# Kernel tuning notes

Measured on AMD Instinct MI355X. Metric: run time of the kernel, lower is better.

The kernel has to match this reference:

```python
import jax, jax.numpy as jnp
import numpy as np
import math

DIM = 256
N = 4096
E = 1024
NEG = -1.0e9


def setup_inputs() -> dict:
    key = jax.random.key(0)
    ks = jax.random.split(key, 10)
    x = jax.random.normal(ks[0], (N, DIM), dtype=jnp.float32)
    # sparse incidence / adjacency (module only uses >0 as mask)
    H = (jax.random.uniform(ks[1], (N, E)) < 0.05).astype(jnp.float32)
    adj = (jax.random.uniform(ks[2], (N, N)) < 0.01).astype(jnp.float32)
    s = 1.0 / math.sqrt(DIM)
    W_he = jax.random.normal(ks[3], (DIM, DIM), dtype=jnp.float32) * s  # HyperedgeAttention.W
    u = jax.random.normal(ks[4], (DIM,), dtype=jnp.float32)            # HyperedgeAttention.u
    W_e = jax.random.normal(ks[5], (DIM, DIM), dtype=jnp.float32) * s  # NodeAttention.W_e
    W_n = jax.random.normal(ks[6], (DIM, DIM), dtype=jnp.float32) * s  # NodeAttention.W_n
    W_g = jax.random.normal(ks[7], (DIM, DIM), dtype=jnp.float32) * s  # GraphAttention.W
    a_g = jax.random.normal(ks[8], (2 * DIM,), dtype=jnp.float32) * s  # GraphAttention.attn weight
    return {"x": x, "H": H, "adj": adj, "W_he": W_he, "u": u,
            "W_e": W_e, "W_n": W_n, "W_g": W_g, "a_g": a_g}


def reference(x, H, adj, W_he, u, W_e, W_n, W_g, a_g):
    n, dim = x.shape
    inv_sqrt_d = 1.0 / math.sqrt(dim)
    maskH = H > 0                       # [N,E] bool
    mask_Hf = maskH.astype(x.dtype)

    # ---- HyperedgeAttention ----
    h_he = x @ W_he                     # [N,dim]
    sc = (h_he @ u) * inv_sqrt_d        # [N]
    scE = jnp.where(maskH, sc[:, None], NEG)      # [N,E]
    A = jax.nn.softmax(scE, axis=0) * mask_Hf     # column softmax over nodes
    e_repr = A.T @ h_he                 # [E,dim]

    # ---- NodeAttention (only B is used) ----
    hn = x @ W_n                        # [N,dim]
    he = e_repr @ W_e                   # [E,dim]
    Bsc = jnp.where(maskH, (hn @ he.T) * inv_sqrt_d, NEG)
    B = jax.nn.softmax(Bsc, axis=1) * mask_Hf     # [N,E]

    # ---- GraphAttention (concat score split: e_ij = lrelu(h_i.a1 + h_j.a2)) ----
    h_g = x @ W_g                       # [N,dim]
    s1 = h_g @ a_g[:dim]                # [N]
    s2 = h_g @ a_g[dim:]                # [N]
    e = jax.nn.leaky_relu(s1[:, None] + s2[None, :], 0.2)   # [N,N]
    maskA = (adj > 0).astype(x.dtype)
    sl = jnp.eye(n, dtype=x.dtype)
    e = e * (maskA + sl) - 1e9 * jnp.clip(1.0 - maskA - sl, 0.0, None)
    G = jax.nn.softmax(e, axis=1)       # [N,N]

    # ---- Mixing ----
    he_sz = jnp.clip(mask_Hf.sum(0), 1.0, None)   # [E]
    M = (G @ mask_Hf) / he_sz[None, :]            # [N,E]
    A_hat = jax.nn.softmax(A.T + M.T, axis=1) * mask_Hf.T   # [E,N]
    e_mix = A_hat @ (x @ W_he)                    # [E,dim]
    B_hat = jax.nn.softmax(B + M, axis=1) * mask_Hf          # [N,E]
    z_h = jax.nn.elu(B_hat @ (e_mix @ W_e))       # [N,dim]
    G_hat = jax.nn.softmax(G + B @ B.T + A @ A.T, axis=1)    # [N,N]
    z_g = jax.nn.elu(G_hat @ (x @ W_g))           # [N,dim]
    return z_h, z_g
```

## Files before the change

### kernel.cpp

```cpp
#include <hip/hip_runtime.h>
#include <math.h>
#include <stdint.h>

#define Nn 4096
#define Ee 1024
#define Dd 256

typedef __attribute__((ext_vector_type(8))) __bf16 bf16x8;
typedef __attribute__((ext_vector_type(4))) float f32x4;
typedef __attribute__((ext_vector_type(8))) unsigned short u16x8;

__device__ __forceinline__ unsigned short f2bf(float f) {
  unsigned int u = __float_as_uint(f);
  unsigned int r = (u + 0x7fffu + ((u >> 16) & 1u)) >> 16;
  return (unsigned short)r;
}
__device__ __forceinline__ float bf2f(unsigned short u) {
  return __uint_as_float(((unsigned int)u) << 16);
}

__device__ __forceinline__ void gload_lds16(const void* g, void* l) {
  __builtin_amdgcn_global_load_lds(
      (__attribute__((address_space(1))) void*)const_cast<void*>(g),
      (__attribute__((address_space(3))) void*)l, 16, 0, 0);
}

__device__ __forceinline__ float block_reduce_sum(float v) {
  __shared__ float sh[4];
  #pragma unroll
  for (int o = 32; o > 0; o >>= 1) v += __shfl_down(v, o);
  int lane = threadIdx.x & 63, w = threadIdx.x >> 6;
  if (lane == 0) sh[w] = v;
  __syncthreads();
  float s = sh[0] + sh[1] + sh[2] + sh[3];
  __syncthreads();
  return s;
}

__global__ __launch_bounds__(256) void gemm_bt_bf16(
    const unsigned short* __restrict__ Ab, const unsigned short* __restrict__ Bb,
    float* __restrict__ Cp, unsigned short* __restrict__ Cb,
    int M, int N, int K, int lda, int ldb, float alpha)
{
  __shared__ unsigned short As[2][128 * 32];
  __shared__ unsigned short Bs[2][128 * 32];
  const int tid = threadIdx.x;
  const int m0 = blockIdx.x * 128, n0 = blockIdx.y * 128;
  const int wave = tid >> 6, lane = tid & 63;
  const int wr = (wave >> 1) * 64, wc = (wave & 1) * 64;
  const int l16 = lane & 15, lq = lane >> 4;
  f32x4 acc[4][4] = {};
  const int NT = K >> 5;

  auto stage = [&](int buf, int kt) {
    const int k0 = kt * 32;
    #pragma unroll
    for (int i = 0; i < 2; ++i) {
      int t2 = tid + i * 256;
      int r = t2 >> 2, c = (t2 & 3) * 8;
      gload_lds16(Ab + (size_t)(m0 + r) * lda + k0 + c, &As[buf][t2 * 8]);
    }
    #pragma unroll
    for (int i = 0; i < 2; ++i) {
      int t2 = tid + i * 256;
      int r = t2 >> 2, c = (t2 & 3) * 8;
      gload_lds16(Bb + (size_t)(n0 + r) * ldb + k0 + c, &Bs[buf][t2 * 8]);
    }
  };

  stage(0, 0);
  __syncthreads();
  int buf = 0;
  for (int kt = 0; kt < NT; ++kt) {
    if (kt + 1 < NT) stage(buf ^ 1, kt + 1);
    bf16x8 af[4], bfr[4];
    #pragma unroll
    for (int m = 0; m < 4; ++m)
      af[m] = *reinterpret_cast<const bf16x8*>(&As[buf][(wr + m * 16 + l16) * 32 + lq * 8]);
    #pragma unroll
    for (int n = 0; n < 4; ++n)
      bfr[n] = *reinterpret_cast<const bf16x8*>(&Bs[buf][(wc + n * 16 + l16) * 32 + lq * 8]);
    #pragma unroll
    for (int m = 0; m < 4; ++m)
      #pragma unroll
      for (int n = 0; n < 4; ++n)
        acc[m][n] = __builtin_amdgcn_mfma_f32_16x16x32_bf16(af[m], bfr[n], acc[m][n], 0, 0, 0);
    __syncthreads();
    buf ^= 1;
  }
  #pragma unroll
  for (int m = 0; m < 4; ++m)
    #pragma unroll
    for (int n = 0; n < 4; ++n) {
      int col = n0 + wc + n * 16 + l16;
      #pragma unroll
      for (int q = 0; q < 4; ++q) {
        int row = m0 + wr + m * 16 + lq * 4 + q;
        size_t idx = (size_t)row * N + col;
        float v = acc[m][n][q] * alpha;
        Cp[idx] = v;
        if (Cb) Cb[idx] = f2bf(v);
      }
    }
}

__global__ __launch_bounds__(256) void gemm_bts_bf16(
    const unsigned short* __restrict__ Ab, const unsigned short* __restrict__ Bb,
    float* __restrict__ Cp, int M, int N, int K, int lda, int ldb, int KS)
{
  __shared__ unsigned short As[2][128 * 32];
  __shared__ unsigned short Bs[2][128 * 32];
  const int tid = threadIdx.x;
  const int m0 = blockIdx.x * 128, n0 = blockIdx.y * 128;
  const int kbase = blockIdx.z * KS;
  const int wave = tid >> 6, lane = tid & 63;
  const int wr = (wave >> 1) * 64, wc = (wave & 1) * 64;
  const int l16 = lane & 15, lq = lane >> 4;
  f32x4 acc[4][4] = {};
  const int NT = KS >> 5;

  auto stage = [&](int buf, int kt) {
    const int k0 = kbase + kt * 32;
    #pragma unroll
    for (int i = 0; i < 2; ++i) {
      int t2 = tid + i * 256;
      int r = t2 >> 2, c = (t2 & 3) * 8;
      gload_lds16(Ab + (size_t)(m0 + r) * lda + k0 + c, &As[buf][t2 * 8]);
    }
    #pragma unroll
    for (int i = 0; i < 2; ++i) {
      int t2 = tid + i * 256;
      int r = t2 >> 2, c = (t2 & 3) * 8;
      gload_lds16(Bb + (size_t)(n0 + r) * ldb + k0 + c, &Bs[buf][t2 * 8]);
    }
  };

  stage(0, 0);
  __syncthreads();
  int buf = 0;
  for (int kt = 0; kt < NT; ++kt) {
    if (kt + 1 < NT) stage(buf ^ 1, kt + 1);
    bf16x8 af[4], bfr[4];
    #pragma unroll
    for (int m = 0; m < 4; ++m)
      af[m] = *reinterpret_cast<const bf16x8*>(&As[buf][(wr + m * 16 + l16) * 32 + lq * 8]);
    #pragma unroll
    for (int n = 0; n < 4; ++n)
      bfr[n] = *reinterpret_cast<const bf16x8*>(&Bs[buf][(wc + n * 16 + l16) * 32 + lq * 8]);
    #pragma unroll
    for (int m = 0; m < 4; ++m)
      #pragma unroll
      for (int n = 0; n < 4; ++n)
        acc[m][n] = __builtin_amdgcn_mfma_f32_16x16x32_bf16(af[m], bfr[n], acc[m][n], 0, 0, 0);
    __syncthreads();
    buf ^= 1;
  }
  #pragma unroll
  for (int m = 0; m < 4; ++m)
    #pragma unroll
    for (int n = 0; n < 4; ++n) {
      int col = n0 + wc + n * 16 + l16;
      #pragma unroll
      for (int q = 0; q < 4; ++q) {
        int row = m0 + wr + m * 16 + lq * 4 + q;
        atomicAdd(&Cp[(size_t)row * N + col], acc[m][n][q]);
      }
    }
}

__global__ __launch_bounds__(256) void gemm_gram_k(
    const unsigned short* __restrict__ CAT,
    unsigned short* __restrict__ Gb,
    float* __restrict__ rowsum)
{
  const int bx = blockIdx.x, by = blockIdx.y;
  if (bx > by) return;
  const int K = 2048;
  __shared__ unsigned short SM[17024];
  unsigned short* Asb = SM;
  unsigned short* Bsb = SM + 8192;
  const int tid = threadIdx.x;
  const int m0 = bx * 128, n0 = by * 128;
  const int wave = tid >> 6, lane = tid & 63;
  const int wr = (wave >> 1) * 64, wc = (wave & 1) * 64;
  const int l16 = lane & 15, lq = lane >> 4;
  f32x4 acc[4][4] = {};
  const int NT = K >> 5;

  auto stage = [&](int buf, int kt) {
    const int k0 = kt * 32;
    #pragma unroll
    for (int i = 0; i < 2; ++i) {
      int t2 = tid + i * 256;
      int r = t2 >> 2, c = (t2 & 3) * 8;
      gload_lds16(CAT + (size_t)(m0 + r) * K + k0 + c, Asb + buf * 4096 + t2 * 8);
    }
    #pragma unroll
    for (int i = 0; i < 2; ++i) {
      int t2 = tid + i * 256;
      int r = t2 >> 2, c = (t2 & 3) * 8;
      gload_lds16(CAT + (size_t)(n0 + r) * K + k0 + c, Bsb + buf * 4096 + t2 * 8);
    }
  };

  stage(0, 0);
  __syncthreads();
  int buf = 0;
  for (int kt = 0; kt < NT; ++kt) {
    if (kt + 1 < NT) stage(buf ^ 1, kt + 1);
    bf16x8 af[4], bfr[4];
    #pragma unroll
    for (int m = 0; m < 4; ++m)
      af[m] = *reinterpret_cast<const bf16x8*>(Asb + buf * 4096 + (wr + m * 16 + l16) * 32 + lq * 8);
    #pragma unroll
    for (int n = 0; n < 4; ++n)
      bfr[n] = *reinterpret_cast<const bf16x8*>(Bsb + buf * 4096 + (wc + n * 16 + l16) * 32 + lq * 8);
    #pragma unroll
    for (int m = 0; m < 4; ++m)
      #pragma unroll
      for (int n = 0; n < 4; ++n)
        acc[m][n] = __builtin_amdgcn_mfma_f32_16x16x32_bf16(af[m], bfr[n], acc[m][n], 0, 0, 0);
    __syncthreads();
    buf ^= 1;
  }
  #pragma unroll
  for (int m = 0; m < 4; ++m)
    #pragma unroll
    for (int q = 0; q < 4; ++q) {
      int row = m0 + wr + m * 16 + lq * 4 + q;
      float s = 0.f;
      #pragma unroll
      for (int n = 0; n < 4; ++n) {
        int col = n0 + wc + n * 16 + l16;
        size_t idx = (size_t)row * Nn + col;
        float e = expf(bf2f(Gb[idx]) + acc[m][n][q]);
        Gb[idx] = f2bf(e);
        s += e;
      }
      s += __shfl_xor(s, 1); s += __shfl_xor(s, 2);
      s += __shfl_xor(s, 4); s += __shfl_xor(s, 8);
      if (l16 == 0) atomicAdd(&rowsum[row], s);
    }
  if (bx == by) return;

  __syncthreads();
  unsigned short* Tg = SM;
  {
    int cc = tid >> 1, r0 = (tid & 1) * 64;
    const unsigned short* src = Gb + (size_t)(n0 + cc) * Nn + m0 + r0;
    unsigned short* dst = Tg + cc * 132 + r0;
    #pragma unroll
    for (int v = 0; v < 8; ++v)
      *reinterpret_cast<u16x8*>(dst + v * 8) = *reinterpret_cast<const u16x8*>(src + v * 8);
  }
  __syncthreads();
  #pragma unroll
  for (int n = 0; n < 4; ++n) {
    int ccl = wc + n * 16 + l16;
    float cs = 0.f;
    #pragma unroll
    for (int m = 0; m < 4; ++m) {
      int sa = ccl * 132 + wr + m * 16 + lq * 4;
      ushort4 lg = *reinterpret_cast<const ushort4*>(&Tg[sa]);
      ushort4 eo;
      float e0 = expf(bf2f(lg.x) + acc[m][n][0]); eo.x = f2bf(e0); cs += e0;
      float e1 = expf(bf2f(lg.y) + acc[m][n][1]); eo.y = f2bf(e1); cs += e1;
      float e2 = expf(bf2f(lg.z) + acc[m][n][2]); eo.z = f2bf(e2); cs += e2;
      float e3 = expf(bf2f(lg.w) + acc[m][n][3]); eo.w = f2bf(e3); cs += e3;
      *reinterpret_cast<ushort4*>(&Tg[sa]) = eo;
    }
    cs += __shfl_xor(cs, 16); cs += __shfl_xor(cs, 32);
    if (lq == 0) atomicAdd(&rowsum[n0 + ccl], cs);
  }
  __syncthreads();
  {
    int cc = tid >> 1, r0 = (tid & 1) * 64;
    const unsigned short* src = Tg + cc * 132 + r0;
    unsigned short* dst = Gb + (size_t)(n0 + cc) * Nn + m0 + r0;
    #pragma unroll
    for (int v = 0; v < 8; ++v)
      *reinterpret_cast<u16x8*>(dst + v * 8) = *reinterpret_cast<const u16x8*>(src + v * 8);
  }
}

__global__ __launch_bounds__(256) void gemm64s_bt_bf16(
    const unsigned short* __restrict__ Ab, const unsigned short* __restrict__ Bb,
    float* __restrict__ Cp, int M, int N, int K, int KS)
{
  __shared__ unsigned short As[2][64 * 64];
  __shared__ unsigned short Bs[2][64 * 64];
  const int tid = threadIdx.x;
  const int m0 = blockIdx.x * 64, n0 = blockIdx.y * 64;
  const int kbase = blockIdx.z * KS;
  const int wave = tid >> 6, lane = tid & 63;
  const int wr = (wave >> 1) * 32, wc = (wave & 1) * 32;
  const int l16 = lane & 15, lq = lane >> 4;
  f32x4 acc[2][2] = {};
  const int NT = KS >> 6;

  auto stage = [&](int buf, int kt) {
    const int k0 = kbase + kt * 64;
    #pragma unroll
    for (int i = 0; i < 2; ++i) {
      int t2 = tid + i * 256;
      int r = t2 >> 3, c = (t2 & 7) * 8;
      gload_lds16(Ab + (size_t)(m0 + r) * K + k0 + c, &As[buf][t2 * 8]);
    }
    #pragma unroll
    for (int i = 0; i < 2; ++i) {
      int t2 = tid + i * 256;
      int r = t2 >> 3, c = (t2 & 7) * 8;
      gload_lds16(Bb + (size_t)(n0 + r) * K + k0 + c, &Bs[buf][t2 * 8]);
    }
  };

  stage(0, 0);
  __syncthreads();
  int buf = 0;
  for (int kt = 0; kt < NT; ++kt) {
    if (kt + 1 < NT) stage(buf ^ 1, kt + 1);
    bf16x8 af[2][2], bfr[2][2];
    #pragma unroll
    for (int m = 0; m < 2; ++m)
      #pragma unroll
      for (int ks = 0; ks < 2; ++ks)
        af[m][ks] = *reinterpret_cast<const bf16x8*>(
            &As[buf][(wr + m * 16 + l16) * 64 + ks * 32 + lq * 8]);
    #pragma unroll
    for (int n = 0; n < 2; ++n)
      #pragma unroll
      for (int ks = 0; ks < 2; ++ks)
        bfr[n][ks] = *reinterpret_cast<const bf16x8*>(
            &Bs[buf][(wc + n * 16 + l16) * 64 + ks * 32 + lq * 8]);
    #pragma unroll
    for (int m = 0; m < 2; ++m)
      #pragma unroll
      for (int n = 0; n < 2; ++n)
        #pragma unroll
        for (int ks = 0; ks < 2; ++ks)
          acc[m][n] = __builtin_amdgcn_mfma_f32_16x16x32_bf16(af[m][ks], bfr[n][ks], acc[m][n], 0, 0, 0);
    __syncthreads();
    buf ^= 1;
  }
  #pragma unroll
  for (int m = 0; m < 2; ++m)
    #pragma unroll
    for (int n = 0; n < 2; ++n) {
      int col = n0 + wc + n * 16 + l16;
      #pragma unroll
      for (int q = 0; q < 4; ++q) {
        int row = m0 + wr + m * 16 + lq * 4 + q;
        atomicAdd(&Cp[(size_t)row * N + col], acc[m][n][q]);
      }
    }
}

__global__ __launch_bounds__(256) void cvt_bf16_k(const float* __restrict__ in,
                                                  unsigned short* __restrict__ out, long n) {
  long i = ((long)blockIdx.x * 256 + threadIdx.x) * 8;
  if (i + 8 > n) return;
  float4 a = *reinterpret_cast<const float4*>(&in[i]);
  float4 b = *reinterpret_cast<const float4*>(&in[i + 4]);
  u16x8 o;
  o[0] = f2bf(a.x); o[1] = f2bf(a.y); o[2] = f2bf(a.z); o[3] = f2bf(a.w);
  o[4] = f2bf(b.x); o[5] = f2bf(b.y); o[6] = f2bf(b.z); o[7] = f2bf(b.w);
  *reinterpret_cast<u16x8*>(&out[i]) = o;
}

__global__ __launch_bounds__(256) void tcvt_k(const float* __restrict__ in,
                                              unsigned short* __restrict__ outT, int R, int S,
                                              const float* __restrict__ coldiv) {
  __shared__ unsigned short tile[64][65];
  int r0 = blockIdx.x * 64, c0 = blockIdx.y * 64;
  int t = threadIdx.x & 63, q = threadIdx.x >> 6;
  float sc = coldiv ? 1.f / fmaxf(coldiv[c0 + t], 1.f) : 1.f;
  for (int rr = q; rr < 64; rr += 4)
    tile[t][rr] = f2bf(in[(long)(r0 + rr) * S + c0 + t] * sc);
  __syncthreads();
  for (int cc = q; cc < 64; cc += 4)
    outT[(long)(c0 + cc) * R + r0 + t] = tile[cc][t];
}

__global__ __launch_bounds__(256) void tcvtW_k(const float* __restrict__ W0,
                                               const float* __restrict__ W1,
                                               const float* __restrict__ W2,
                                               const float* __restrict__ W3,
                                               unsigned short* __restrict__ outT) {
  __shared__ unsigned short tile[64][65];
  int s = blockIdx.z;
  const float* in = s == 0 ? W0 : (s == 1 ? W1 : (s == 2 ? W2 : W3));
  unsigned short* o = outT + (size_t)s * 256 * 256;
  int r0 = blockIdx.x * 64, c0 = blockIdx.y * 64;
  int t = threadIdx.x & 63, q = threadIdx.x >> 6;
  for (int rr = q; rr < 64; rr += 4)
    tile[t][rr] = f2bf(in[(long)(r0 + rr) * Dd + c0 + t]);
  __syncthreads();
  for (int cc = q; cc < 64; cc += 4)
    o[(long)(c0 + cc) * Dd + r0 + t] = tile[cc][t];
}

__global__ __launch_bounds__(256) void tcvtH_k(const float* __restrict__ hcat4,
                                               unsigned short* __restrict__ hWT,
                                               unsigned short* __restrict__ hgT) {
  __shared__ unsigned short tile[64][65];
  int s = blockIdx.z;
  const float* in = hcat4 + (s == 0 ? 768 : 512);
  unsigned short* o = s == 0 ? hWT : hgT;
  int r0 = blockIdx.x * 64, c0 = blockIdx.y * 64;
  int t = threadIdx.x & 63, q = threadIdx.x >> 6;
  for (int rr = q; rr < 64; rr += 4)
    tile[t][rr] = f2bf(in[(long)(r0 + rr) * 1024 + c0 + t]);
  __syncthreads();
  for (int cc = q; cc < 64; cc += 4)
    o[(long)(c0 + cc) * Nn + r0 + t] = tile[cc][t];
}

__global__ __launch_bounds__(256) void elu_rows_k(float* __restrict__ p,
                                                  const float* __restrict__ rowsum) {
  long i = ((long)blockIdx.x * 256 + threadIdx.x) * 4;
  float4 v = *reinterpret_cast<const float4*>(&p[i]);
  float sc = 1.f;
  long half = (long)Nn * Dd;
  if (i >= half) sc = 1.f / rowsum[(i - half) >> 8];
  v.x *= sc; v.y *= sc; v.z *= sc; v.w *= sc;
  v.x = v.x > 0.f ? v.x : expm1f(v.x);
  v.y = v.y > 0.f ? v.y : expm1f(v.y);
  v.z = v.z > 0.f ? v.z : expm1f(v.z);
  v.w = v.w > 0.f ? v.w : expm1f(v.w);
  *reinterpret_cast<float4*>(&p[i]) = v;
}

__global__ __launch_bounds__(256) void gemm64_k(
    const float* __restrict__ Ap, const float* __restrict__ Bp, float* __restrict__ Cp,
    int M, int N, int K, int Asm, int Ask, int Bsk, int Bsn)
{
  __shared__ alignas(16) float As[16][68];
  __shared__ alignas(16) float Bs[16][68];
  const int tid = threadIdx.x;
  const int tx = tid & 15, ty = tid >> 4;
  const int m0 = blockIdx.x * 64, n0 = blockIdx.y * 64;
  float acc[4][4] = {};
  for (int k0 = 0; k0 < K; k0 += 16) {
    if (Ask == 1) {
      int mm = tid >> 2, kk = (tid & 3) << 2;
      float4 v = *reinterpret_cast<const float4*>(&Ap[(long)(m0 + mm) * Asm + k0 + kk]);
      As[kk + 0][mm] = v.x; As[kk + 1][mm] = v.y; As[kk + 2][mm] = v.z; As[kk + 3][mm] = v.w;
    } else {
      int kk = tid >> 4, mm = (tid & 15) << 2;
      *reinterpret_cast<float4*>(&As[kk][mm]) =
          *reinterpret_cast<const float4*>(&Ap[(long)(k0 + kk) * Ask + m0 + mm]);
    }
    if (Bsn == 1) {
      int kk = tid >> 4, nn = (tid & 15) << 2;
      *reinterpret_cast<float4*>(&Bs[kk][nn]) =
          *reinterpret_cast<const float4*>(&Bp[(long)(k0 + kk) * Bsk + n0 + nn]);
    } else {
      int nn = tid >> 2, kk = (tid & 3) << 2;
      float4 v = *reinterpret_cast<const float4*>(&Bp[(long)(n0 + nn) * Bsn + k0 + kk]);
      Bs[kk + 0][nn] = v.x; Bs[kk + 1][nn] = v.y; Bs[kk + 2][nn] = v.z; Bs[kk + 3][nn] = v.w;
    }
    __syncthreads();
    #pragma unroll
    for (int kk = 0; kk < 16; ++kk) {
      float4 av = *reinterpret_cast<const float4*>(&As[kk][ty << 2]);
      float4 bv = *reinterpret_cast<const float4*>(&Bs[kk][tx << 2]);
      float a[4] = {av.x, av.y, av.z, av.w};
      float b[4] = {bv.x, bv.y, bv.z, bv.w};
      #pragma unroll
      for (int r = 0; r < 4; ++r)
        #pragma unroll
        for (int c = 0; c < 4; ++c) acc[r][c] = fmaf(a[r], b[c], acc[r][c]);
    }
    __syncthreads();
  }
  #pragma unroll
  for (int r = 0; r < 4; ++r) {
    long base = (long)(m0 + (ty << 2) + r) * N + n0 + (tx << 2);
    float4 o = {acc[r][0], acc[r][1], acc[r][2], acc[r][3]};
    *reinterpret_cast<float4*>(&Cp[base]) = o;
  }
}

__global__ __launch_bounds__(256) void rowdots_k(
    const float* __restrict__ hcat, const float* __restrict__ u, const float* __restrict__ a_g,
    float* __restrict__ esc, float* __restrict__ s1, float* __restrict__ s2)
{
  int i = blockIdx.x, t = threadIdx.x;
  float hh = hcat[(long)i * 1024 + t];
  float hg = hcat[(long)i * 1024 + 512 + t];
  float d0 = block_reduce_sum(hh * u[t]);
  float d1 = block_reduce_sum(hg * a_g[t]);
  float d2 = block_reduce_sum(hg * a_g[Dd + t]);
  if (t == 0) {
    esc[i] = expf(d0 * 0.0625f);
    s1[i] = d1;
    s2[i] = d2;
  }
}

__global__ __launch_bounds__(256) void colstats_k(
    const float* __restrict__ H, const float* __restrict__ esc,
    float* __restrict__ colden, float* __restrict__ cnt)
{
  int e = blockIdx.x * 256 + threadIdx.x;
  int r0 = blockIdx.y * 128;
  float d = 0.f, c = 0.f;
  for (int r = r0; r < r0 + 128; ++r) {
    float h = H[(long)r * Ee + e];
    if (h > 0.f) { d += esc[r]; c += 1.f; }
  }
  atomicAdd(&colden[e], d);
  atomicAdd(&cnt[e], c);
}

__global__ __launch_bounds__(256) void fillA_k(
    const float* __restrict__ H, const float* __restrict__ esc,
    const float* __restrict__ colden,
    unsigned short* __restrict__ CAT, unsigned short* __restrict__ AbT)
{
  __shared__ unsigned short tile[64][68];
  int r0 = blockIdx.x * 64, e0 = blockIdx.y * 64;
  int te = threadIdx.x & 63, tq = threadIdx.x >> 6;
  float cd = colden[e0 + te];
  for (int rr = tq; rr < 64; rr += 4) {
    long idx = (long)(r0 + rr) * Ee + e0 + te;
    float h = H[idx];
    float val = h > 0.f ? esc[r0 + rr] / cd : 0.f;
    unsigned short vb = f2bf(val);
    CAT[(long)(r0 + rr) * 2048 + 1024 + e0 + te] = vb;
    tile[te][rr] = vb;
  }
  __syncthreads();
  for (int ee = tq; ee < 64; ee += 4)
    AbT[(long)(e0 + ee) * Nn + r0 + te] = tile[ee][te];
}

__global__ __launch_bounds__(256) void brow_k(const float* __restrict__ Bbuf,
                                              const float* __restrict__ H,
                                              unsigned short* __restrict__ CAT)
{
  int i = blockIdx.x, t = threadIdx.x;
  long base = (long)i * Ee + t * 4;
  float4 raw = *reinterpret_cast<const float4*>(&Bbuf[base]);
  float4 h = *reinterpret_cast<const float4*>(&H[base]);
  float rr[4] = {raw.x, raw.y, raw.z, raw.w}, hh[4] = {h.x, h.y, h.z, h.w};
  float p[4]; float s = 0.f;
  #pragma unroll
  for (int k = 0; k < 4; ++k) { p[k] = hh[k] > 0.f ? expf(rr[k]) : 0.f; s += p[k]; }
  float den = block_reduce_sum(s);
  float inv = den > 0.f ? 1.f / den : 0.f;
  ushort4 ob = {f2bf(p[0] * inv), f2bf(p[1] * inv), f2bf(p[2] * inv), f2bf(p[3] * inv)};
  *reinterpret_cast<ushort4*>(&CAT[(long)i * 2048 + t * 4]) = ob;
}

__global__ __launch_bounds__(256) void gfill_k(
    const float* __restrict__ adj, const float* __restrict__ s1,
    const float* __restrict__ s2, unsigned short* __restrict__ Gb)
{
  int i = blockIdx.x, t = threadIdx.x;
  float s1i = s1[i];
  float p[16]; float sum = 0.f;
  #pragma unroll
  for (int c = 0; c < 4; ++c) {
    int j = c * 1024 + t * 4;
    float4 a = *reinterpret_cast<const float4*>(&adj[(long)i * Nn + j]);
    float4 sv = *reinterpret_cast<const float4*>(&s2[j]);
    float aa[4] = {a.x, a.y, a.z, a.w}, ss[4] = {sv.x, sv.y, sv.z, sv.w};
    #pragma unroll
    for (int k = 0; k < 4; ++k) {
      float f = (aa[k] > 0.f ? 1.f : 0.f) + ((j + k) == i ? 1.f : 0.f);
      float l = s1i + ss[k];
      l = l > 0.f ? l : 0.2f * l;
      float val = l * f - 1e9f * fmaxf(1.f - f, 0.f);
      float pp = expf(val);
      p[c * 4 + k] = pp; sum += pp;
    }
  }
  float den = block_reduce_sum(sum);
  float inv = 1.f / den;
  #pragma unroll
  for (int c = 0; c < 4; ++c) {
    int j = c * 1024 + t * 4;
    ushort4 ob = {f2bf(p[c * 4] * inv), f2bf(p[c * 4 + 1] * inv),
                  f2bf(p[c * 4 + 2] * inv), f2bf(p[c * 4 + 3] * inv)};
    *reinterpret_cast<ushort4*>(&Gb[(long)i * Nn + j]) = ob;
  }
}

__global__ __launch_bounds__(256) void amstats_k(
    const unsigned short* __restrict__ CAT, const float* __restrict__ Mm,
    float* __restrict__ aden)
{
  int e = blockIdx.x * 256 + threadIdx.x;
  int r0 = blockIdx.y * 128;
  float d = 0.f;
  for (int r = r0; r < r0 + 128; ++r)
    d += expf(bf2f(CAT[(size_t)r * 2048 + 1024 + e]) + Mm[(size_t)r * Ee + e]);
  atomicAdd(&aden[e], d);
}

__global__ __launch_bounds__(256) void ahat_k(
    const unsigned short* __restrict__ CAT, const float* __restrict__ Mm,
    const float* __restrict__ H, const float* __restrict__ aden,
    unsigned short* __restrict__ AhB)
{
  __shared__ float tile[64][65];
  int j0 = blockIdx.x * 64, e0 = blockIdx.y * 64;
  int te = threadIdx.x & 63;
  int tq = threadIdx.x >> 6;
  int e = e0 + te;
  float inv = 1.f / aden[e];
  for (int jj = tq; jj < 64; jj += 4) {
    long idx = (long)(j0 + jj) * Ee + e;
    float a = bf2f(CAT[(size_t)(j0 + jj) * 2048 + 1024 + e]);
    float val = (H[idx] > 0.f) ? expf(a + Mm[idx]) * inv : 0.f;
    tile[te][jj] = val;
  }
  __syncthreads();
  for (int ee = tq; ee < 64; ee += 4)
    AhB[(long)(e0 + ee) * Nn + j0 + te] = f2bf(tile[ee][te]);
}

__global__ __launch_bounds__(256) void bhat_k(const unsigned short* __restrict__ CAT,
                                              const float* __restrict__ Mm,
                                              const float* __restrict__ H,
                                              unsigned short* __restrict__ Bb2)
{
  int i = blockIdx.x, t = threadIdx.x;
  long base = (long)i * Ee + t * 4;
  ushort4 bu = *reinterpret_cast<const ushort4*>(&CAT[(long)i * 2048 + t * 4]);
  float4 m = *reinterpret_cast<const float4*>(&Mm[base]);
  float4 h = *reinterpret_cast<const float4*>(&H[base]);
  float bb[4] = {bf2f(bu.x), bf2f(bu.y), bf2f(bu.z), bf2f(bu.w)};
  float mm2[4] = {m.x, m.y, m.z, m.w}, hh[4] = {h.x, h.y, h.z, h.w};
  float p[4]; float s = 0.f;
  #pragma unroll
  for (int k = 0; k < 4; ++k) { p[k] = expf(bb[k] + mm2[k]); s += p[k]; }
  float den = block_reduce_sum(s);
  float inv = 1.f / den;
  #pragma unroll
  for (int k = 0; k < 4; ++k) p[k] = hh[k] > 0.f ? p[k] * inv : 0.f;
  ushort4 ob = {f2bf(p[0]), f2bf(p[1]), f2bf(p[2]), f2bf(p[3])};
  *reinterpret_cast<ushort4*>(&Bb2[base]) = ob;
}

extern "C" void kernel_launch(void* const* d_in, const int* in_sizes, int n_in,
                              void* d_out, int out_size, void* d_ws, size_t ws_size,
                              hipStream_t stream) {
  const float* x    = (const float*)d_in[0];
  const float* H    = (const float*)d_in[1];
  const float* adj  = (const float*)d_in[2];
  const float* W_he = (const float*)d_in[3];
  const float* u    = (const float*)d_in[4];
  const float* W_e  = (const float*)d_in[5];
  const float* W_n  = (const float*)d_in[6];
  const float* W_g  = (const float*)d_in[7];
  const float* a_g  = (const float*)d_in[8];
  float* out = (float*)d_out;
  float* ws  = (float*)d_ws;
  (void)in_sizes; (void)n_in; (void)out_size; (void)ws_size;

  size_t off = 0;
  auto alloc = [&](size_t n) { float* p = ws + off; off += n; return p; };
  float* hcat4  = alloc((size_t)Nn * 1024);
  float* Wp     = alloc((size_t)Dd * Dd);
  float* esc    = alloc(Nn);
  float* s1     = alloc(Nn);
  float* s2     = alloc(Nn);
  float* colden = alloc(Ee);
  float* cnt    = alloc(Ee);
  float* aden   = alloc(Ee);
  float* rowsum = alloc(Nn);
  float* heb    = alloc((size_t)Ee * Dd);
  float* tewTf  = alloc((size_t)Dd * Ee);
  float* Bbuf   = alloc((size_t)Nn * Ee);
  float* Mm     = alloc((size_t)Nn * Ee);
  unsigned short* Gb    = (unsigned short*)alloc((size_t)Nn * Nn / 2);
  unsigned short* CAT   = (unsigned short*)alloc((size_t)Nn * 2048 / 2);
  unsigned short* Hbt   = (unsigned short*)alloc((size_t)Ee * Nn / 2);
  unsigned short* AbT   = (unsigned short*)alloc((size_t)Ee * Nn / 2);
  unsigned short* AhB   = (unsigned short*)alloc((size_t)Ee * Nn / 2);
  unsigned short* hWT   = (unsigned short*)alloc((size_t)Dd * Nn / 2);
  unsigned short* hgT   = (unsigned short*)alloc((size_t)Dd * Nn / 2);
  unsigned short* tewT  = (unsigned short*)alloc((size_t)Dd * Ee / 2);
  unsigned short* Bb2   = (unsigned short*)alloc((size_t)Nn * Ee / 2);
  unsigned short* xb    = (unsigned short*)alloc((size_t)Nn * Dd / 2);
  unsigned short* WcTb4 = (unsigned short*)alloc((size_t)1024 * Dd / 2);
  unsigned short* hcatB = (unsigned short*)alloc((size_t)Nn * 1024 / 2);
  unsigned short* hebB  = (unsigned short*)alloc((size_t)Ee * Dd / 2);

  hipMemsetAsync(colden, 0, (3 * Ee + Nn) * sizeof(float), stream);
  hipMemsetAsync(heb, 0, 2 * (size_t)Ee * Dd * sizeof(float), stream);
  hipMemsetAsync(Mm, 0, (size_t)Nn * Ee * sizeof(float), stream);
  hipMemsetAsync(out, 0, 2 * (size_t)Nn * Dd * sizeof(float), stream);

  auto gbt = [&](const unsigned short* A, const unsigned short* B, float* C, unsigned short* Cb,
                 int M, int N, int K, int lda, int ldb, float alpha) {
    gemm_bt_bf16<<<dim3(M / 128, N / 128), 256, 0, stream>>>(A, B, C, Cb, M, N, K, lda, ldb, alpha);
  };
  auto gbts = [&](const unsigned short* A, const unsigned short* B, float* C,
                  int M, int N, int K, int lda, int ldb, int KS) {
    gemm_bts_bf16<<<dim3(M / 128, N / 128, K / KS), 256, 0, stream>>>(A, B, C, M, N, K, lda, ldb, KS);
  };
  auto gs64 = [&](const unsigned short* A, const unsigned short* B, float* C,
                  int M, int N, int K, int KS) {
    gemm64s_bt_bf16<<<dim3(M / 64, N / 64, K / KS), 256, 0, stream>>>(A, B, C, M, N, K, KS);
  };
  auto tcvt = [&](const float* in, unsigned short* o, int R, int S, int cols, const float* cd) {
    tcvt_k<<<dim3(R / 64, cols / 64), 256, 0, stream>>>(in, o, R, S, cd);
  };

  gemm64_k<<<dim3(4, 4), 256, 0, stream>>>(W_he, W_e, Wp, Dd, Dd, Dd, Dd, 1, Dd, 1);
  cvt_bf16_k<<<(Nn * Dd) / 2048, 256, 0, stream>>>(x, xb, (long)Nn * Dd);
  tcvtW_k<<<dim3(4, 4, 4), 256, 0, stream>>>(W_he, W_n, W_g, Wp, WcTb4);
  gbt(xb, WcTb4, hcat4, hcatB, Nn, 1024, Dd, Dd, Dd, 1.f);
  rowdots_k<<<Nn, 256, 0, stream>>>(hcat4, u, a_g, esc, s1, s2);
  tcvtH_k<<<dim3(Nn / 64, Dd / 64, 2), 256, 0, stream>>>(hcat4, hWT, hgT);
  colstats_k<<<dim3(Ee / 256, 32), 256, 0, stream>>>(H, esc, colden, cnt);
  fillA_k<<<dim3(Nn / 64, Ee / 64), 256, 0, stream>>>(H, esc, colden, CAT, AbT);
  gs64(AbT, hWT, heb, Ee, Dd, Nn, 512);
  cvt_bf16_k<<<(Ee * Dd) / 2048, 256, 0, stream>>>(heb, hebB, (long)Ee * Dd);
  gbt(hcatB + 256, hebB, Bbuf, nullptr, Nn, Ee, Dd, 1024, Dd, 0.0625f);
  brow_k<<<Nn, 256, 0, stream>>>(Bbuf, H, CAT);
  gfill_k<<<Nn, 256, 0, stream>>>(adj, s1, s2, Gb);
  tcvt(H, Hbt, Nn, Ee, Ee, cnt);
  gbts(Gb, Hbt, Mm, Nn, Ee, Nn, Nn, Nn, 2048);
  gemm_gram_k<<<dim3(32, 32), 256, 0, stream>>>(CAT, Gb, rowsum);
  amstats_k<<<dim3(Ee / 256, 32), 256, 0, stream>>>(CAT, Mm, aden);
  ahat_k<<<dim3(Nn / 64, Ee / 64), 256, 0, stream>>>(CAT, Mm, H, aden, AhB);
  gs64(hWT, AhB, tewTf, Dd, Ee, Nn, 512);
  cvt_bf16_k<<<(Dd * Ee) / 2048, 256, 0, stream>>>(tewTf, tewT, (long)Dd * Ee);
  bhat_k<<<Nn, 256, 0, stream>>>(CAT, Mm, H, Bb2);
  gs64(Bb2, tewT, out, Nn, Dd, Ee, 512);
  gbts(Gb, hgT, out + (size_t)Nn * Dd, Nn, Dd, Nn, Nn, Nn, 512);
  elu_rows_k<<<(2 * Nn * Dd) / 1024, 256, 0, stream>>>(out, rowsum);
}
```

Measured before the change: 592.2 us.

## Merge independent GEMMs into combined launches and defer softmax normalisations

The G@H GEMM and the Gram/exp kernel now run in one launch, using separate z-slices and a separate Gexp output buffer so that Gb stays readable. The z_g GEMM and the hWT·AhB GEMM are likewise packed into one launch. The A-hat and B-hat softmax denominators are no longer applied in place. They are folded into a tew conversion (division by aden) and into the final ELU scaling (bden), and a new expbm kernel computes B-hat and the A column sums in a single pass. The aim is fewer launches and fewer serialized stages, with better GPU fill from co-scheduling. The cost is an extra N×N bf16 buffer and a heavier expbm block loop.

```diff
diff --git a/kernel.cpp b/kernel.cpp
--- a/kernel.cpp
+++ b/kernel.cpp
@@ -35,6 +35,215 @@
   float s = sh[0] + sh[1] + sh[2] + sh[3];
   __syncthreads();
   return s;
+}
+
+__device__ __forceinline__ void bts_dev(
+    const unsigned short* __restrict__ Ab, const unsigned short* __restrict__ Bb,
+    float* __restrict__ Cp, int N, int lda, int ldb,
+    int m0, int n0, int kbase, int NT, unsigned short* SM)
+{
+  unsigned short* As = SM;
+  unsigned short* Bs = SM + 8192;
+  const int tid = threadIdx.x;
+  const int wave = tid >> 6, lane = tid & 63;
+  const int wr = (wave >> 1) * 64, wc = (wave & 1) * 64;
+  const int l16 = lane & 15, lq = lane >> 4;
+  f32x4 acc[4][4] = {};
+
+  auto stage = [&](int buf, int kt) {
+    const int k0 = kbase + kt * 32;
+    #pragma unroll
+    for (int i = 0; i < 2; ++i) {
+      int t2 = tid + i * 256;
+      int r = t2 >> 2, c = (t2 & 3) * 8;
+      gload_lds16(Ab + (size_t)(m0 + r) * lda + k0 + c, As + buf * 4096 + t2 * 8);
+    }
+    #pragma unroll
+    for (int i = 0; i < 2; ++i) {
+      int t2 = tid + i * 256;
+      int r = t2 >> 2, c = (t2 & 3) * 8;
+      gload_lds16(Bb + (size_t)(n0 + r) * ldb + k0 + c, Bs + buf * 4096 + t2 * 8);
+    }
+  };
+
+  stage(0, 0);
+  __syncthreads();
+  int buf = 0;
+  for (int kt = 0; kt < NT; ++kt) {
+    if (kt + 1 < NT) stage(buf ^ 1, kt + 1);
+    bf16x8 af[4], bfr[4];
+    #pragma unroll
+    for (int m = 0; m < 4; ++m)
+      af[m] = *reinterpret_cast<const bf16x8*>(As + buf * 4096 + (wr + m * 16 + l16) * 32 + lq * 8);
+    #pragma unroll
+    for (int n = 0; n < 4; ++n)
+      bfr[n] = *reinterpret_cast<const bf16x8*>(Bs + buf * 4096 + (wc + n * 16 + l16) * 32 + lq * 8);
+    #pragma unroll
+    for (int m = 0; m < 4; ++m)
+      #pragma unroll
+      for (int n = 0; n < 4; ++n)
+        acc[m][n] = __builtin_amdgcn_mfma_f32_16x16x32_bf16(af[m], bfr[n], acc[m][n], 0, 0, 0);
+    __syncthreads();
+    buf ^= 1;
+  }
+  #pragma unroll
+  for (int m = 0; m < 4; ++m)
+    #pragma unroll
+    for (int n = 0; n < 4; ++n) {
+      int col = n0 + wc + n * 16 + l16;
+      #pragma unroll
+      for (int q = 0; q < 4; ++q) {
+        int row = m0 + wr + m * 16 + lq * 4 + q;
+        atomicAdd(&Cp[(size_t)row * N + col], acc[m][n][q]);
+      }
+    }
+}
+
+__device__ __forceinline__ void gram_dev(
+    const unsigned short* __restrict__ CAT, const unsigned short* __restrict__ Gb,
+    unsigned short* __restrict__ Gexp, float* __restrict__ rowsum,
+    int bx, int by, unsigned short* SM)
+{
+  const int K = 2048;
+  unsigned short* Asb = SM;
+  unsigned short* Bsb = SM + 8192;
+  const int tid = threadIdx.x;
+  const int m0 = bx * 128, n0 = by * 128;
+  const int wave = tid >> 6, lane = tid & 63;
+  const int wr = (wave >> 1) * 64, wc = (wave & 1) * 64;
+  const int l16 = lane & 15, lq = lane >> 4;
+  f32x4 acc[4][4] = {};
+  const int NT = K >> 5;
+
+  auto stage = [&](int buf, int kt) {
+    const int k0 = kt * 32;
+    #pragma unroll
+    for (int i = 0; i < 2; ++i) {
+      int t2 = tid + i * 256;
+      int r = t2 >> 2, c = (t2 & 3) * 8;
+      gload_lds16(CAT + (size_t)(m0 + r) * K + k0 + c, Asb + buf * 4096 + t2 * 8);
+    }
+    #pragma unroll
+    for (int i = 0; i < 2; ++i) {
+      int t2 = tid + i * 256;
+      int r = t2 >> 2, c = (t2 & 3) * 8;
+      gload_lds16(CAT + (size_t)(n0 + r) * K + k0 + c, Bsb + buf * 4096 + t2 * 8);
+    }
+  };
+
+  stage(0, 0);
+  __syncthreads();
+  int buf = 0;
+  for (int kt = 0; kt < NT; ++kt) {
+    if (kt + 1 < NT) stage(buf ^ 1, kt + 1);
+    bf16x8 af[4], bfr[4];
+    #pragma unroll
+    for (int m = 0; m < 4; ++m)
+      af[m] = *reinterpret_cast<const bf16x8*>(Asb + buf * 4096 + (wr + m * 16 + l16) * 32 + lq * 8);
+    #pragma unroll
+    for (int n = 0; n < 4; ++n)
+      bfr[n] = *reinterpret_cast<const bf16x8*>(Bsb + buf * 4096 + (wc + n * 16 + l16) * 32 + lq * 8);
+    #pragma unroll
+    for (int m = 0; m < 4; ++m)
+      #pragma unroll
+      for (int n = 0; n < 4; ++n)
+        acc[m][n] = __builtin_amdgcn_mfma_f32_16x16x32_bf16(af[m], bfr[n], acc[m][n], 0, 0, 0);
+    __syncthreads();
+    buf ^= 1;
+  }
+  #pragma unroll
+  for (int m = 0; m < 4; ++m)
+    #pragma unroll
+    for (int q = 0; q < 4; ++q) {
+      int row = m0 + wr + m * 16 + lq * 4 + q;
+      float s = 0.f;
+      #pragma unroll
+      for (int n = 0; n < 4; ++n) {
+        int col = n0 + wc + n * 16 + l16;
+        size_t idx = (size_t)row * Nn + col;
+        float e = expf(bf2f(Gb[idx]) + acc[m][n][q]);
+        Gexp[idx] = f2bf(e);
+        s += e;
+      }
+      s += __shfl_xor(s, 1); s += __shfl_xor(s, 2);
+      s += __shfl_xor(s, 4); s += __shfl_xor(s, 8);
+      if (l16 == 0) atomicAdd(&rowsum[row], s);
+    }
+  if (bx == by) return;
+
+  __syncthreads();
+  unsigned short* Tg = SM;
+  {
+    int cc = tid >> 1, r0 = (tid & 1) * 64;
+    const unsigned short* src = Gb + (size_t)(n0 + cc) * Nn + m0 + r0;
+    unsigned short* dst = Tg + cc * 132 + r0;
+    #pragma unroll
+    for (int v = 0; v < 8; ++v)
+      *reinterpret_cast<u16x8*>(dst + v * 8) = *reinterpret_cast<const u16x8*>(src + v * 8);
+  }
+  __syncthreads();
+  #pragma unroll
+  for (int n = 0; n < 4; ++n) {
+    int ccl = wc + n * 16 + l16;
+    float cs = 0.f;
+    #pragma unroll
+    for (int m = 0; m < 4; ++m) {
+      int sa = ccl * 132 + wr + m * 16 + lq * 4;
+      ushort4 lg = *reinterpret_cast<const ushort4*>(&Tg[sa]);
+      ushort4 eo;
+      float e0 = expf(bf2f(lg.x) + acc[m][n][0]); eo.x = f2bf(e0); cs += e0;
+      float e1 = expf(bf2f(lg.y) + acc[m][n][1]); eo.y = f2bf(e1); cs += e1;
+      float e2 = expf(bf2f(lg.z) + acc[m][n][2]); eo.z = f2bf(e2); cs += e2;
+      float e3 = expf(bf2f(lg.w) + acc[m][n][3]); eo.w = f2bf(e3); cs += e3;
+      *reinterpret_cast<ushort4*>(&Tg[sa]) = eo;
+    }
+    cs += __shfl_xor(cs, 16); cs += __shfl_xor(cs, 32);
+    if (lq == 0) atomicAdd(&rowsum[n0 + ccl], cs);
+  }
+  __syncthreads();
+  {
+    int cc = tid >> 1, r0 = (tid & 1) * 64;
+    const unsigned short* src = Tg + cc * 132 + r0;
+    unsigned short* dst = Gexp + (size_t)(n0 + cc) * Nn + m0 + r0;
+    #pragma unroll
+    for (int v = 0; v < 8; ++v)
+      *reinterpret_cast<u16x8*>(dst + v * 8) = *reinterpret_cast<const u16x8*>(src + v * 8);
+  }
+}
+
+__global__ __launch_bounds__(256) void mgram_k(
+    const unsigned short* __restrict__ CAT, const unsigned short* __restrict__ Gb,
+    unsigned short* __restrict__ Gexp, float* __restrict__ rowsum,
+    const unsigned short* __restrict__ Hbt, float* __restrict__ Mm)
+{
+  __shared__ unsigned short SM[17024];
+  if (blockIdx.z == 0) {
+    if (blockIdx.x > blockIdx.y) return;
+    gram_dev(CAT, Gb, Gexp, rowsum, blockIdx.x, blockIdx.y, SM);
+  } else {
+    int m0 = blockIdx.x * 128;
+    int n0 = (blockIdx.y & 7) * 128;
+    int kbase = (blockIdx.y >> 3) * 1024;
+    bts_dev(Gb, Hbt, Mm, Ee, Nn, Nn, m0, n0, kbase, 32, SM);
+  }
+}
+
+__global__ __launch_bounds__(256) void zgtew_k(
+    const unsigned short* __restrict__ Gexp, const unsigned short* __restrict__ hgT,
+    float* __restrict__ outzg,
+    const unsigned short* __restrict__ hWT, const unsigned short* __restrict__ AhB,
+    float* __restrict__ tewTf)
+{
+  __shared__ unsigned short SM[16384];
+  int z = blockIdx.z;
+  if (z < 8) {
+    bts_dev(Gexp, hgT, outzg, Dd, Nn, Nn, blockIdx.x * 128, blockIdx.y * 128, z * 512, 16, SM);
+  } else {
+    int linear = (z - 8) * 64 + blockIdx.y * 32 + blockIdx.x;
+    int tile = linear & 15, ks = linear >> 4;
+    int m0 = (tile >> 3) * 128, n0 = (tile & 7) * 128;
+    bts_dev(hWT, AhB, tewTf, Ee, Nn, Nn, m0, n0, ks * 512, 16, SM);
+  }
 }
 
 __global__ __launch_bounds__(256) void gemm_bt_bf16(
@@ -102,185 +311,6 @@
         if (Cb) Cb[idx] = f2bf(v);
       }
     }
-}
-
-__global__ __launch_bounds__(256) void gemm_bts_bf16(
-    const unsigned short* __restrict__ Ab, const unsigned short* __restrict__ Bb,
-    float* __restrict__ Cp, int M, int N, int K, int lda, int ldb, int KS)
-{
-  __shared__ unsigned short As[2][128 * 32];
-  __shared__ unsigned short Bs[2][128 * 32];
-  const int tid = threadIdx.x;
-  const int m0 = blockIdx.x * 128, n0 = blockIdx.y * 128;
-  const int kbase = blockIdx.z * KS;
-  const int wave = tid >> 6, lane = tid & 63;
-  const int wr = (wave >> 1) * 64, wc = (wave & 1) * 64;
-  const int l16 = lane & 15, lq = lane >> 4;
-  f32x4 acc[4][4] = {};
-  const int NT = KS >> 5;
-
-  auto stage = [&](int buf, int kt) {
-    const int k0 = kbase + kt * 32;
-    #pragma unroll
-    for (int i = 0; i < 2; ++i) {
-      int t2 = tid + i * 256;
-      int r = t2 >> 2, c = (t2 & 3) * 8;
-      gload_lds16(Ab + (size_t)(m0 + r) * lda + k0 + c, &As[buf][t2 * 8]);
-    }
-    #pragma unroll
-    for (int i = 0; i < 2; ++i) {
-      int t2 = tid + i * 256;
-      int r = t2 >> 2, c = (t2 & 3) * 8;
-      gload_lds16(Bb + (size_t)(n0 + r) * ldb + k0 + c, &Bs[buf][t2 * 8]);
-    }
-  };
-
-  stage(0, 0);
-  __syncthreads();
-  int buf = 0;
-  for (int kt = 0; kt < NT; ++kt) {
-    if (kt + 1 < NT) stage(buf ^ 1, kt + 1);
-    bf16x8 af[4], bfr[4];
-    #pragma unroll
-    for (int m = 0; m < 4; ++m)
-      af[m] = *reinterpret_cast<const bf16x8*>(&As[buf][(wr + m * 16 + l16) * 32 + lq * 8]);
-    #pragma unroll
-    for (int n = 0; n < 4; ++n)
-      bfr[n] = *reinterpret_cast<const bf16x8*>(&Bs[buf][(wc + n * 16 + l16) * 32 + lq * 8]);
-    #pragma unroll
-    for (int m = 0; m < 4; ++m)
-      #pragma unroll
-      for (int n = 0; n < 4; ++n)
-        acc[m][n] = __builtin_amdgcn_mfma_f32_16x16x32_bf16(af[m], bfr[n], acc[m][n], 0, 0, 0);
-    __syncthreads();
-    buf ^= 1;
-  }
-  #pragma unroll
-  for (int m = 0; m < 4; ++m)
-    #pragma unroll
-    for (int n = 0; n < 4; ++n) {
-      int col = n0 + wc + n * 16 + l16;
-      #pragma unroll
-      for (int q = 0; q < 4; ++q) {
-        int row = m0 + wr + m * 16 + lq * 4 + q;
-        atomicAdd(&Cp[(size_t)row * N + col], acc[m][n][q]);
-      }
-    }
-}
-
-__global__ __launch_bounds__(256) void gemm_gram_k(
-    const unsigned short* __restrict__ CAT,
-    unsigned short* __restrict__ Gb,
-    float* __restrict__ rowsum)
-{
-  const int bx = blockIdx.x, by = blockIdx.y;
-  if (bx > by) return;
-  const int K = 2048;
-  __shared__ unsigned short SM[17024];
-  unsigned short* Asb = SM;
-  unsigned short* Bsb = SM + 8192;
-  const int tid = threadIdx.x;
-  const int m0 = bx * 128, n0 = by * 128;
-  const int wave = tid >> 6, lane = tid & 63;
-  const int wr = (wave >> 1) * 64, wc = (wave & 1) * 64;
-  const int l16 = lane & 15, lq = lane >> 4;
-  f32x4 acc[4][4] = {};
-  const int NT = K >> 5;
-
-  auto stage = [&](int buf, int kt) {
-    const int k0 = kt * 32;
-    #pragma unroll
-    for (int i = 0; i < 2; ++i) {
-      int t2 = tid + i * 256;
-      int r = t2 >> 2, c = (t2 & 3) * 8;
-      gload_lds16(CAT + (size_t)(m0 + r) * K + k0 + c, Asb + buf * 4096 + t2 * 8);
-    }
-    #pragma unroll
-    for (int i = 0; i < 2; ++i) {
-      int t2 = tid + i * 256;
-      int r = t2 >> 2, c = (t2 & 3) * 8;
-      gload_lds16(CAT + (size_t)(n0 + r) * K + k0 + c, Bsb + buf * 4096 + t2 * 8);
-    }
-  };
-
-  stage(0, 0);
-  __syncthreads();
-  int buf = 0;
-  for (int kt = 0; kt < NT; ++kt) {
-    if (kt + 1 < NT) stage(buf ^ 1, kt + 1);
-    bf16x8 af[4], bfr[4];
-    #pragma unroll
-    for (int m = 0; m < 4; ++m)
-      af[m] = *reinterpret_cast<const bf16x8*>(Asb + buf * 4096 + (wr + m * 16 + l16) * 32 + lq * 8);
-    #pragma unroll
-    for (int n = 0; n < 4; ++n)
-      bfr[n] = *reinterpret_cast<const bf16x8*>(Bsb + buf * 4096 + (wc + n * 16 + l16) * 32 + lq * 8);
-    #pragma unroll
-    for (int m = 0; m < 4; ++m)
-      #pragma unroll
-      for (int n = 0; n < 4; ++n)
-        acc[m][n] = __builtin_amdgcn_mfma_f32_16x16x32_bf16(af[m], bfr[n], acc[m][n], 0, 0, 0);
-    __syncthreads();
-    buf ^= 1;
-  }
-  #pragma unroll
-  for (int m = 0; m < 4; ++m)
-    #pragma unroll
-    for (int q = 0; q < 4; ++q) {
-      int row = m0 + wr + m * 16 + lq * 4 + q;
-      float s = 0.f;
-      #pragma unroll
-      for (int n = 0; n < 4; ++n) {
-        int col = n0 + wc + n * 16 + l16;
-        size_t idx = (size_t)row * Nn + col;
-        float e = expf(bf2f(Gb[idx]) + acc[m][n][q]);
-        Gb[idx] = f2bf(e);
-        s += e;
-      }
-      s += __shfl_xor(s, 1); s += __shfl_xor(s, 2);
-      s += __shfl_xor(s, 4); s += __shfl_xor(s, 8);
-      if (l16 == 0) atomicAdd(&rowsum[row], s);
-    }
-  if (bx == by) return;
-
-  __syncthreads();
-  unsigned short* Tg = SM;
-  {
-    int cc = tid >> 1, r0 = (tid & 1) * 64;
-    const unsigned short* src = Gb + (size_t)(n0 + cc) * Nn + m0 + r0;
-    unsigned short* dst = Tg + cc * 132 + r0;
-    #pragma unroll
-    for (int v = 0; v < 8; ++v)
-      *reinterpret_cast<u16x8*>(dst + v * 8) = *reinterpret_cast<const u16x8*>(src + v * 8);
-  }
-  __syncthreads();
-  #pragma unroll
-  for (int n = 0; n < 4; ++n) {
-    int ccl = wc + n * 16 + l16;
-    float cs = 0.f;
-    #pragma unroll
-    for (int m = 0; m < 4; ++m) {
-      int sa = ccl * 132 + wr + m * 16 + lq * 4;
-      ushort4 lg = *reinterpret_cast<const ushort4*>(&Tg[sa]);
-      ushort4 eo;
-      float e0 = expf(bf2f(lg.x) + acc[m][n][0]); eo.x = f2bf(e0); cs += e0;
-      float e1 = expf(bf2f(lg.y) + acc[m][n][1]); eo.y = f2bf(e1); cs += e1;
-      float e2 = expf(bf2f(lg.z) + acc[m][n][2]); eo.z = f2bf(e2); cs += e2;
-      float e3 = expf(bf2f(lg.w) + acc[m][n][3]); eo.w = f2bf(e3); cs += e3;
-      *reinterpret_cast<ushort4*>(&Tg[sa]) = eo;
-    }
-    cs += __shfl_xor(cs, 16); cs += __shfl_xor(cs, 32);
-    if (lq == 0) atomicAdd(&rowsum[n0 + ccl], cs);
-  }
-  __syncthreads();
-  {
-    int cc = tid >> 1, r0 = (tid & 1) * 64;
-    const unsigned short* src = Tg + cc * 132 + r0;
-    unsigned short* dst = Gb + (size_t)(n0 + cc) * Nn + m0 + r0;
-    #pragma unroll
-    for (int v = 0; v < 8; ++v)
-      *reinterpret_cast<u16x8*>(dst + v * 8) = *reinterpret_cast<const u16x8*>(src + v * 8);
-  }
 }
 
 __global__ __launch_bounds__(256) void gemm64s_bt_bf16(
@@ -364,6 +394,21 @@
   u16x8 o;
   o[0] = f2bf(a.x); o[1] = f2bf(a.y); o[2] = f2bf(a.z); o[3] = f2bf(a.w);
   o[4] = f2bf(b.x); o[5] = f2bf(b.y); o[6] = f2bf(b.z); o[7] = f2bf(b.w);
+  *reinterpret_cast<u16x8*>(&out[i]) = o;
+}
+
+__global__ __launch_bounds__(256) void cvt_cs_k(const float* __restrict__ in,
+                                                unsigned short* __restrict__ out,
+                                                const float* __restrict__ aden) {
+  long i = ((long)blockIdx.x * 256 + threadIdx.x) * 8;
+  int e0 = (int)(i & 1023);
+  float4 a = *reinterpret_cast<const float4*>(&in[i]);
+  float4 b = *reinterpret_cast<const float4*>(&in[i + 4]);
+  float4 d0 = *reinterpret_cast<const float4*>(&aden[e0]);
+  float4 d1 = *reinterpret_cast<const float4*>(&aden[e0 + 4]);
+  u16x8 o;
+  o[0] = f2bf(a.x / d0.x); o[1] = f2bf(a.y / d0.y); o[2] = f2bf(a.z / d0.z); o[3] = f2bf(a.w / d0.w);
+  o[4] = f2bf(b.x / d1.x); o[5] = f2bf(b.y / d1.y); o[6] = f2bf(b.z / d1.z); o[7] = f2bf(b.w / d1.w);
   *reinterpret_cast<u16x8*>(&out[i]) = o;
 }
 
@@ -416,12 +461,12 @@
 }
 
 __global__ __launch_bounds__(256) void elu_rows_k(float* __restrict__ p,
+                                                  const float* __restrict__ bden,
                                                   const float* __restrict__ rowsum) {
   long i = ((long)blockIdx.x * 256 + threadIdx.x) * 4;
   float4 v = *reinterpret_cast<const float4*>(&p[i]);
-  float sc = 1.f;
   long half = (long)Nn * Dd;
-  if (i >= half) sc = 1.f / rowsum[(i - half) >> 8];
+  float sc = (i < half) ? 1.f / bden[i >> 8] : 1.f / rowsum[(i - half) >> 8];
   v.x *= sc; v.y *= sc; v.z *= sc; v.w *= sc;
   v.x = v.x > 0.f ? v.x : expm1f(v.x);
   v.y = v.y > 0.f ? v.y : expm1f(v.y);
@@ -587,61 +632,59 @@
   }
 }
 
-__global__ __launch_bounds__(256) void amstats_k(
+__global__ __launch_bounds__(256) void expbm_k(
     const unsigned short* __restrict__ CAT, const float* __restrict__ Mm,
-    float* __restrict__ aden)
-{
-  int e = blockIdx.x * 256 + threadIdx.x;
-  int r0 = blockIdx.y * 128;
-  float d = 0.f;
-  for (int r = r0; r < r0 + 128; ++r)
-    d += expf(bf2f(CAT[(size_t)r * 2048 + 1024 + e]) + Mm[(size_t)r * Ee + e]);
-  atomicAdd(&aden[e], d);
+    const float* __restrict__ H, unsigned short* __restrict__ Bb2,
+    float* __restrict__ bden, float* __restrict__ aden)
+{
+  int t = threadIdx.x;
+  int i0 = blockIdx.x * 16;
+  float pa[4] = {0.f, 0.f, 0.f, 0.f};
+  for (int r = 0; r < 16; ++r) {
+    int i = i0 + r;
+    long base = (long)i * Ee + t * 4;
+    ushort4 bu = *reinterpret_cast<const ushort4*>(&CAT[(long)i * 2048 + t * 4]);
+    ushort4 au = *reinterpret_cast<const ushort4*>(&CAT[(long)i * 2048 + 1024 + t * 4]);
+    float4 m = *reinterpret_cast<const float4*>(&Mm[base]);
+    float4 h = *reinterpret_cast<const float4*>(&H[base]);
+    float mm[4] = {m.x, m.y, m.z, m.w}, hh[4] = {h.x, h.y, h.z, h.w};
+    unsigned short bs[4] = {bu.x, bu.y, bu.z, bu.w}, as[4] = {au.x, au.y, au.z, au.w};
+    float eb[4]; float s = 0.f;
+    #pragma unroll
+    for (int k = 0; k < 4; ++k) {
+      eb[k] = expf(bf2f(bs[k]) + mm[k]); s += eb[k];
+      pa[k] += expf(bf2f(as[k]) + mm[k]);
+    }
+    float den = block_reduce_sum(s);
+    ushort4 ob = {hh[0] > 0.f ? f2bf(eb[0]) : (unsigned short)0,
+                  hh[1] > 0.f ? f2bf(eb[1]) : (unsigned short)0,
+                  hh[2] > 0.f ? f2bf(eb[2]) : (unsigned short)0,
+                  hh[3] > 0.f ? f2bf(eb[3]) : (unsigned short)0};
+    *reinterpret_cast<ushort4*>(&Bb2[base]) = ob;
+    if (t == 0) bden[i] = den;
+  }
+  #pragma unroll
+  for (int k = 0; k < 4; ++k) atomicAdd(&aden[t * 4 + k], pa[k]);
 }
 
 __global__ __launch_bounds__(256) void ahat_k(
     const unsigned short* __restrict__ CAT, const float* __restrict__ Mm,
-    const float* __restrict__ H, const float* __restrict__ aden,
-    unsigned short* __restrict__ AhB)
+    const float* __restrict__ H, unsigned short* __restrict__ AhB)
 {
   __shared__ float tile[64][65];
   int j0 = blockIdx.x * 64, e0 = blockIdx.y * 64;
   int te = threadIdx.x & 63;
   int tq = threadIdx.x >> 6;
   int e = e0 + te;
-  float inv = 1.f / aden[e];
   for (int jj = tq; jj < 64; jj += 4) {
     long idx = (long)(j0 + jj) * Ee + e;
     float a = bf2f(CAT[(size_t)(j0 + jj) * 2048 + 1024 + e]);
-    float val = (H[idx] > 0.f) ? expf(a + Mm[idx]) * inv : 0.f;
+    float val = (H[idx] > 0.f) ? expf(a + Mm[idx]) : 0.f;
     tile[te][jj] = val;
   }
   __syncthreads();
   for (int ee = tq; ee < 64; ee += 4)
     AhB[(long)(e0 + ee) * Nn + j0 + te] = f2bf(tile[ee][te]);
-}
-
-__global__ __launch_bounds__(256) void bhat_k(const unsigned short* __restrict__ CAT,
-                                              const float* __restrict__ Mm,
-                                              const float* __restrict__ H,
-                                              unsigned short* __restrict__ Bb2)
-{
-  int i = blockIdx.x, t = threadIdx.x;
-  long base = (long)i * Ee + t * 4;
-  ushort4 bu = *reinterpret_cast<const ushort4*>(&CAT[(long)i * 2048 + t * 4]);
-  float4 m = *reinterpret_cast<const float4*>(&Mm[base]);
-  float4 h = *reinterpret_cast<const float4*>(&H[base]);
-  float bb[4] = {bf2f(bu.x), bf2f(bu.y), bf2f(bu.z), bf2f(bu.w)};
-  float mm2[4] = {m.x, m.y, m.z, m.w}, hh[4] = {h.x, h.y, h.z, h.w};
-  float p[4]; float s = 0.f;
-  #pragma unroll
-  for (int k = 0; k < 4; ++k) { p[k] = expf(bb[k] + mm2[k]); s += p[k]; }
-  float den = block_reduce_sum(s);
-  float inv = 1.f / den;
-  #pragma unroll
-  for (int k = 0; k < 4; ++k) p[k] = hh[k] > 0.f ? p[k] * inv : 0.f;
-  ushort4 ob = {f2bf(p[0]), f2bf(p[1]), f2bf(p[2]), f2bf(p[3])};
-  *reinterpret_cast<ushort4*>(&Bb2[base]) = ob;
 }
 
 extern "C" void kernel_launch(void* const* d_in, const int* in_sizes, int n_in,
@@ -671,11 +714,13 @@
   float* cnt    = alloc(Ee);
   float* aden   = alloc(Ee);
   float* rowsum = alloc(Nn);
+  float* bden   = alloc(Nn);
   float* heb    = alloc((size_t)Ee * Dd);
   float* tewTf  = alloc((size_t)Dd * Ee);
   float* Bbuf   = alloc((size_t)Nn * Ee);
   float* Mm     = alloc((size_t)Nn * Ee);
   unsigned short* Gb    = (unsigned short*)alloc((size_t)Nn * Nn / 2);
+  unsigned short* Gexp  = (unsigned short*)alloc((size_t)Nn * Nn / 2);
   unsigned short* CAT   = (unsigned short*)alloc((size_t)Nn * 2048 / 2);
   unsigned short* Hbt   = (unsigned short*)alloc((size_t)Ee * Nn / 2);
   unsigned short* AbT   = (unsigned short*)alloc((size_t)Ee * Nn / 2);
@@ -689,7 +734,7 @@
   unsigned short* hcatB = (unsigned short*)alloc((size_t)Nn * 1024 / 2);
   unsigned short* hebB  = (unsigned short*)alloc((size_t)Ee * Dd / 2);
 
-  hipMemsetAsync(colden, 0, (3 * Ee + Nn) * sizeof(float), stream);
+  hipMemsetAsync(colden, 0, (3 * Ee + 2 * Nn) * sizeof(float), stream);
   hipMemsetAsync(heb, 0, 2 * (size_t)Ee * Dd * sizeof(float), stream);
   hipMemsetAsync(Mm, 0, (size_t)Nn * Ee * sizeof(float), stream);
   hipMemsetAsync(out, 0, 2 * (size_t)Nn * Dd * sizeof(float), stream);
@@ -697,10 +742,6 @@
   auto gbt = [&](const unsigned short* A, const unsigned short* B, float* C, unsigned short* Cb,
                  int M, int N, int K, int lda, int ldb, float alpha) {
     gemm_bt_bf16<<<dim3(M / 128, N / 128), 256, 0, stream>>>(A, B, C, Cb, M, N, K, lda, ldb, alpha);
-  };
-  auto gbts = [&](const unsigned short* A, const unsigned short* B, float* C,
-                  int M, int N, int K, int lda, int ldb, int KS) {
-    gemm_bts_bf16<<<dim3(M / 128, N / 128, K / KS), 256, 0, stream>>>(A, B, C, M, N, K, lda, ldb, KS);
   };
   auto gs64 = [&](const unsigned short* A, const unsigned short* B, float* C,
                   int M, int N, int K, int KS) {
@@ -724,14 +765,11 @@
   brow_k<<<Nn, 256, 0, stream>>>(Bbuf, H, CAT);
   gfill_k<<<Nn, 256, 0, stream>>>(adj, s1, s2, Gb);
   tcvt(H, Hbt, Nn, Ee, Ee, cnt);
-  gbts(Gb, Hbt, Mm, Nn, Ee, Nn, Nn, Nn, 2048);
-  gemm_gram_k<<<dim3(32, 32), 256, 0, stream>>>(CAT, Gb, rowsum);
-  amstats_k<<<dim3(Ee / 256, 32), 256, 0, stream>>>(CAT, Mm, aden);
-  ahat_k<<<dim3(Nn / 64, Ee / 64), 256, 0, stream>>>(CAT, Mm, H, aden, AhB);
-  gs64(hWT, AhB, tewTf, Dd, Ee, Nn, 512);
-  cvt_bf16_k<<<(Dd * Ee) / 2048, 256, 0, stream>>>(tewTf, tewT, (long)Dd * Ee);
-  bhat_k<<<Nn, 256, 0, stream>>>(CAT, Mm, H, Bb2);
+  mgram_k<<<dim3(32, 32, 2), 256, 0, stream>>>(CAT, Gb, Gexp, rowsum, Hbt, Mm);
+  expbm_k<<<256, 256, 0, stream>>>(CAT, Mm, H, Bb2, bden, aden);
+  ahat_k<<<dim3(Nn / 64, Ee / 64), 256, 0, stream>>>(CAT, Mm, H, AhB);
+  zgtew_k<<<dim3(32, 2, 10), 256, 0, stream>>>(Gexp, hgT, out + (size_t)Nn * Dd, hWT, AhB, tewTf);
+  cvt_cs_k<<<(Dd * Ee) / 2048, 256, 0, stream>>>(tewTf, tewT, aden);
   gs64(Bb2, tewT, out, Nn, Dd, Ee, 512);
-  gbts(Gb, hgT, out + (size_t)Nn * Dd, Nn, Dd, Nn, Nn, Nn, 512);
-  elu_rows_k<<<(2 * Nn * Dd) / 1024, 256, 0, stream>>>(out, rowsum);
-}
+  elu_rows_k<<<(2 * Nn * Dd) / 1024, 256, 0, stream>>>(out, bden, rowsum);
+}
```

New measurement: 595.0 us. About the same (+0.5%).
